# Kernel tuning notes

Measured on AMD Instinct MI355X. Metric: run time of the kernel, lower is better.

Reference implementation:

```python
import jax, jax.numpy as jnp
import numpy as np

N, E, G = 20480, 163840, 512          # nodes, edges, graphs
D, H, R, L = 128, 4, 8, 4             # embed dim, heads, relations, layers
HK = H * D                            # heads * out_channels (RGATConv internal width)
BOARD_WIDTH = 7
NEG_SLOPE = 0.2                       # RGATConv leaky_relu slope


def setup_inputs() -> dict:
    key = jax.random.key(0)
    ks = jax.random.split(key, 12)
    s_in = 1.0 / np.sqrt(D)
    s_att = 1.0 / np.sqrt(HK)
    return {
        "x_nodes": jax.random.randint(ks[0], (N,), 0, 3),
        "edge_index": jax.random.randint(ks[1], (2, E), 0, N),
        "edge_type": jax.random.randint(ks[2], (E,), 0, R),
        "batch": jnp.arange(N) // (N // G),  # G graphs of N//G nodes each
        "emb": jax.random.normal(ks[3], (3, D), jnp.float32),
        "W": jax.random.normal(ks[4], (L, R, D, HK), jnp.float32) * s_in,
        "Q": jax.random.normal(ks[5], (L, HK, H), jnp.float32) * s_att,
        "K": jax.random.normal(ks[6], (L, HK, H), jnp.float32) * s_att,
        "B": jnp.zeros((L, D), jnp.float32),
        "fc1_w": jax.random.normal(ks[7], (D, 64), jnp.float32) * s_in,
        "fc1_b": jnp.zeros((64,), jnp.float32),
        "pol_w": jax.random.normal(ks[8], (64, BOARD_WIDTH), jnp.float32) * 0.125,
        "pol_b": jnp.zeros((BOARD_WIDTH,), jnp.float32),
        "val_w": jax.random.normal(ks[9], (64, 1), jnp.float32) * 0.125,
        "val_b": jnp.zeros((1,), jnp.float32),
    }


def _rgat_layer(x, W, Q, Km, b, src, dst, etype):
    # RGATConv, additive-self-attention, across-relation softmax, concat=False.
    x_all = jnp.einsum('nd,rdk->nrk', x, W)          # [N,R,HK] per-relation transform
    q_all = jnp.einsum('nrk,kh->nrh', x_all, Q)      # [N,R,H]
    k_all = jnp.einsum('nrk,kh->nrh', x_all, Km)     # [N,R,H]
    alpha = jax.nn.leaky_relu(q_all[dst, etype] + k_all[src, etype], NEG_SLOPE)  # [E,H]
    # segment softmax over destination nodes (across all relations)
    amax = jax.lax.stop_gradient(jax.ops.segment_max(alpha, dst, num_segments=N))
    ex = jnp.exp(alpha - amax[dst])
    denom = jax.ops.segment_sum(ex, dst, num_segments=N)
    a = ex / (denom[dst] + 1e-16)                    # [E,H]
    msg = x_all[src, etype].reshape(E, H, D) * a[:, :, None]   # [E,H,D]
    agg = jax.ops.segment_sum(msg.reshape(E, HK), dst, num_segments=N)
    out = agg.reshape(N, H, D).mean(axis=1) + b      # head-mean (concat=False) + bias
    return jax.nn.relu(out)


def reference(x_nodes, edge_index, edge_type, batch, emb, W, Q, K, B,
              fc1_w, fc1_b, pol_w, pol_b, val_w, val_b):
    src, dst = edge_index[0], edge_index[1]
    x = emb[x_nodes]                                  # [N,D]
    for l in range(L):
        x = _rgat_layer(x, W[l], Q[l], K[l], B[l], src, dst, edge_type)
    cnt = jax.ops.segment_sum(jnp.ones((N,), x.dtype), batch, num_segments=G)
    pooled = jax.ops.segment_sum(x, batch, num_segments=G) / jnp.maximum(cnt, 1.0)[:, None]
    h = jax.nn.relu(pooled @ fc1_w + fc1_b)           # [G,64]
    policy = h @ pol_w + pol_b                        # [G,BOARD_WIDTH]
    value = jnp.tanh(h @ val_w + val_b)               # [G,1]
    return policy, value
```

## Files before the change

### kernel.cpp

```cpp
#include <hip/hip_runtime.h>
#include <cstdint>
#include <cstddef>

constexpr int N_  = 20480;
constexpr int E_  = 163840;
constexpr int G_  = 512;
constexpr int D_  = 128;
constexpr int H_  = 4;
constexpr int R_  = 8;
constexpr int L_  = 4;
constexpr int HK_ = 512;
constexpr int NPG_ = N_ / G_;

typedef short short8 __attribute__((ext_vector_type(8)));
typedef float f32x4 __attribute__((ext_vector_type(4)));
typedef unsigned short u16;
typedef unsigned int u32;

__device__ inline u16 bfr(float f) {
  u32 u = __builtin_bit_cast(u32, f);
  return (u16)((u + 0x7fffu + ((u >> 16) & 1u)) >> 16);
}
__device__ inline float bf2f(u32 lo16) { return __builtin_bit_cast(float, lo16 << 16); }
__device__ inline float lrelu(float v) { return v >= 0.f ? v : 0.2f * v; }

__global__ void k_zero_i(int* __restrict__ p, int n) {
  int i = blockIdx.x * blockDim.x + threadIdx.x;
  if (i < n) p[i] = 0;
}

__global__ void k_count_rel(const int* __restrict__ dst, const int* __restrict__ et,
                            int* __restrict__ counts) {
  int e = blockIdx.x * blockDim.x + threadIdx.x;
  if (e < E_) atomicAdd(&counts[et[e] * N_ + dst[e]], 1);
}
__global__ void k_count_dst(const int* __restrict__ dst, int* __restrict__ counts) {
  int e = blockIdx.x * blockDim.x + threadIdx.x;
  if (e < E_) atomicAdd(&counts[dst[e]], 1);
}
__global__ void k_bsum(const int* __restrict__ c, int* __restrict__ bsum) {
  int t = threadIdx.x;
  const int4 v = *(const int4*)&c[blockIdx.x * 1024 + t * 4];
  int s = v.x + v.y + v.z + v.w;
#pragma unroll
  for (int o = 32; o; o >>= 1) s += __shfl_down(s, o, 64);
  __shared__ int ws_[4];
  if ((t & 63) == 0) ws_[t >> 6] = s;
  __syncthreads();
  if (t == 0) bsum[blockIdx.x] = ws_[0] + ws_[1] + ws_[2] + ws_[3];
}
__global__ void k_bscan(int* __restrict__ bsum, int nb, int* __restrict__ tot_out) {
  __shared__ int sh[512];
  int t = threadIdx.x;
  if (t < nb) sh[t] = bsum[t];
  __syncthreads();
  if (t == 0) {
    int run = 0;
    for (int i = 0; i < nb; ++i) { int v = sh[i]; sh[i] = run; run += v; }
    tot_out[0] = run;
  }
  __syncthreads();
  if (t < nb) bsum[t] = sh[t];
}
__global__ void k_scan3(const int* __restrict__ c, const int* __restrict__ bsum,
                        int* __restrict__ indptr, int* __restrict__ cursor) {
  __shared__ int ts[256];
  int t = threadIdx.x;
  int base = blockIdx.x * 1024 + t * 4;
  const int4 v = *(const int4*)&c[base];
  int s0 = v.x, s01 = v.x + v.y, s012 = s01 + v.z, s = s012 + v.w;
  ts[t] = s;
  __syncthreads();
#pragma unroll
  for (int o = 1; o < 256; o <<= 1) {
    int add = (t >= o) ? ts[t - o] : 0;
    __syncthreads();
    ts[t] += add;
    __syncthreads();
  }
  int off = bsum[blockIdx.x] + (t ? ts[t - 1] : 0);
  int4 o4 = make_int4(off, off + s0, off + s01, off + s012);
  *(int4*)&indptr[base] = o4;
  *(int4*)&cursor[base] = o4;
}
__global__ void k_scatter_rel(const int* __restrict__ dst, const int* __restrict__ et,
                              const int* __restrict__ src, int* __restrict__ cursor,
                              int* __restrict__ esort, int* __restrict__ slotOf,
                              int* __restrict__ srcR) {
  int e = blockIdx.x * blockDim.x + threadIdx.x;
  if (e < E_) {
    int p = atomicAdd(&cursor[et[e] * N_ + dst[e]], 1);
    esort[p] = e;
    slotOf[e] = p;
    srcR[p] = src[e];
  }
}
__global__ void k_scatter_dst(const int* __restrict__ dst, int* __restrict__ cursor,
                              int* __restrict__ esort) {
  int e = blockIdx.x * blockDim.x + threadIdx.x;
  if (e < E_) {
    int p = atomicAdd(&cursor[dst[e]], 1);
    esort[p] = e;
  }
}
__global__ void k_padbase(const int* __restrict__ indptrR, int* __restrict__ padBase) {
  if (threadIdx.x == 0 && blockIdx.x == 0) {
    int cum = 0;
    for (int r = 0; r < R_; ++r) {
      padBase[r] = cum;
      int cnt = indptrR[(r + 1) * N_] - indptrR[r * N_];
      cum += (cnt + 63) & ~63;
    }
    padBase[R_] = cum;
  }
}

__global__ void k_embed(const int* __restrict__ xn, const float* __restrict__ emb,
                        float* __restrict__ x, u16* __restrict__ xb) {
  int i = blockIdx.x * blockDim.x + threadIdx.x;
  if (i < N_ * D_) {
    int n = i >> 7, d = i & 127;
    float v = emb[xn[n] * D_ + d];
    x[i] = v;
    xb[i] = bfr(v);
  }
}

__global__ __launch_bounds__(256) void k_wqk_all(const float* __restrict__ W,
                                                 const float* __restrict__ Q,
                                                 const float* __restrict__ Km,
                                                 float* __restrict__ WQK) {
  int gw = (blockIdx.x * 256 + threadIdx.x) >> 6;
  int lane = threadIdx.x & 63;
  int d = gw & 127, r = (gw >> 7) & 7, l = gw >> 10;
  const float* wrow = W + (((size_t)l * R_ + r) * D_ + d) * HK_;
  const float* Ql = Q + (size_t)l * HK_ * H_;
  const float* Kl = Km + (size_t)l * HK_ * H_;
  float acc[8] = {0.f, 0.f, 0.f, 0.f, 0.f, 0.f, 0.f, 0.f};
#pragma unroll
  for (int it = 0; it < 8; ++it) {
    int k = it * 64 + lane;
    float w = wrow[k];
    const float4 qv = *(const float4*)&Ql[k * 4];
    const float4 kv = *(const float4*)&Kl[k * 4];
    acc[0] += w * qv.x; acc[1] += w * qv.y; acc[2] += w * qv.z; acc[3] += w * qv.w;
    acc[4] += w * kv.x; acc[5] += w * kv.y; acc[6] += w * kv.z; acc[7] += w * kv.w;
  }
#pragma unroll
  for (int o = 32; o; o >>= 1)
#pragma unroll
    for (int j = 0; j < 8; ++j) acc[j] += __shfl_down(acc[j], o, 64);
  if (lane == 0) {
#pragma unroll
    for (int h = 0; h < 4; ++h) {
      WQK[((size_t)l * D_ + d) * 64 + r * 4 + h] = acc[h];
      WQK[((size_t)l * D_ + d) * 64 + 32 + r * 4 + h] = acc[4 + h];
    }
  }
}

__global__ __launch_bounds__(256) void k_qk(const float* __restrict__ x,
                                            const float* __restrict__ WQK,
                                            float* __restrict__ q,
                                            float* __restrict__ kk) {
  __shared__ float xs[32][129];
  __shared__ float wq[128][64];
  const int t = threadIdx.x;
  const int n0 = blockIdx.x * 32;
#pragma unroll
  for (int p = 0; p < 4; ++p) {
    int idx = t + p * 256;
    int row = idx >> 5, c4 = (idx & 31) * 4;
    const float4 v = *(const float4*)&x[(size_t)(n0 + row) * D_ + c4];
    xs[row][c4 + 0] = v.x; xs[row][c4 + 1] = v.y;
    xs[row][c4 + 2] = v.z; xs[row][c4 + 3] = v.w;
  }
#pragma unroll
  for (int p = 0; p < 8; ++p) {
    int idx = t + p * 256;
    int row = idx >> 4, c4 = (idx & 15) * 4;
    *(float4*)&wq[row][c4] = *(const float4*)&WQK[row * 64 + c4];
  }
  __syncthreads();
  const int node = t >> 3, cq = t & 7;
  float s[8];
#pragma unroll
  for (int j = 0; j < 8; ++j) s[j] = 0.f;
  for (int k = 0; k < 128; ++k) {
    float xv = xs[node][k];
#pragma unroll
    for (int j = 0; j < 8; ++j) s[j] = fmaf(xv, wq[k][cq * 8 + j], s[j]);
  }
#pragma unroll
  for (int j = 0; j < 8; ++j) {
    int c = cq * 8 + j;
    if (c < 32) q[(size_t)(n0 + node) * 32 + c] = s[j];
    else        kk[(size_t)(n0 + node) * 32 + (c - 32)] = s[j];
  }
}

__global__ __launch_bounds__(256) void k_attn(
    const int* __restrict__ ipN, const int* __restrict__ esD,
    const int* __restrict__ src, const int* __restrict__ et,
    const float* __restrict__ q, const float* __restrict__ kk,
    const int* __restrict__ slotOf, float* __restrict__ aw) {
  int n = blockIdx.x * 4 + (threadIdx.x >> 6);
  int lane = threadIdx.x & 63;
  int j0 = ipN[n], j1 = ipN[n + 1];
  int deg = j1 - j0;
  if (deg == 0) return;
  int h = lane & 3;
  int nch = (deg + 15) >> 4;
  float m = -3.4e38f;
  for (int c = 0; c < nch; ++c) {
    int ei = c * 16 + (lane >> 2);
    if (ei < deg) {
      int e = esD[j0 + ei];
      int r = et[e];
      float a = lrelu(q[(size_t)n * 32 + r * 4 + h] + kk[(size_t)src[e] * 32 + r * 4 + h]);
      m = fmaxf(m, a);
    }
  }
#pragma unroll
  for (int o = 4; o < 64; o <<= 1) m = fmaxf(m, __shfl_xor(m, o, 64));
  float s = 0.f;
  for (int c = 0; c < nch; ++c) {
    int ei = c * 16 + (lane >> 2);
    if (ei < deg) {
      int e = esD[j0 + ei];
      int r = et[e];
      float a = lrelu(q[(size_t)n * 32 + r * 4 + h] + kk[(size_t)src[e] * 32 + r * 4 + h]);
      float ex = expf(a - m);
      s += ex;
      aw[(size_t)slotOf[e] * 4 + h] = ex;
    }
  }
#pragma unroll
  for (int o = 4; o < 64; o <<= 1) s += __shfl_xor(s, o, 64);
  float inv = 0.25f / (s + 1e-16f);
  for (int c = 0; c < nch; ++c) {
    int ei = c * 16 + (lane >> 2);
    if (ei < deg) {
      int e = esD[j0 + ei];
      aw[(size_t)slotOf[e] * 4 + h] *= inv;
    }
  }
}

__global__ void k_cvt_w_all(const float* __restrict__ W, u16* __restrict__ wt) {
  __shared__ u16 tile[64][65];
  const int z = blockIdx.z, k0 = blockIdx.y * 64, c0 = blockIdx.x * 64;
  const int t = threadIdx.x;
  const int tk = t >> 4, tc4 = (t & 15) * 4;
  const float* Wz = W + (size_t)z * D_ * HK_;
  u16* wz = wt + (size_t)z * HK_ * D_;
#pragma unroll
  for (int p = 0; p < 4; ++p) {
    int krow = tk + p * 16;
    const float4 v = *(const float4*)&Wz[(size_t)(k0 + krow) * HK_ + c0 + tc4];
    tile[tc4 + 0][krow] = bfr(v.x);
    tile[tc4 + 1][krow] = bfr(v.y);
    tile[tc4 + 2][krow] = bfr(v.z);
    tile[tc4 + 3][krow] = bfr(v.w);
  }
  __syncthreads();
#pragma unroll
  for (int p = 0; p < 4; ++p) {
    int crow = tk + p * 16;
    uint2 o;
    o.x = (u32)tile[crow][tc4 + 0] | ((u32)tile[crow][tc4 + 1] << 16);
    o.y = (u32)tile[crow][tc4 + 2] | ((u32)tile[crow][tc4 + 3] << 16);
    *(uint2*)&wz[(size_t)(c0 + crow) * D_ + k0 + tc4] = o;
  }
}

__global__ __launch_bounds__(512, 2) void k_edge4(
    const u16* __restrict__ xb, const u16* __restrict__ wt,
    const int* __restrict__ indptrR, const int* __restrict__ padBase,
    const int* __restrict__ srcR, const float* __restrict__ aw,
    u16* __restrict__ m) {
  __shared__ u16 atile[64 * 128];
  __shared__ float awl[2][64][4];
  __shared__ int srcl[2][64];
  const int t = threadIdx.x;
  const int r = blockIdx.x >> 5;
  const int sub = blockIdx.x & 31;
  const int ip0 = indptrR[r * N_];
  const int cnt = indptrR[(r + 1) * N_] - ip0;
  const int nt = (cnt + 63) >> 6;
  const int pb = padBase[r];
  const u16* wrp = wt + (size_t)r * HK_ * D_;
  const int wid = t >> 6, lane = t & 63;
  const int l15 = lane & 15, l4 = lane >> 4;
  short8 breg[4][4];
#pragma unroll
  for (int ks = 0; ks < 4; ++ks)
#pragma unroll
    for (int h = 0; h < 4; ++h) {
      int c = (wid + 8 * h) * 16 + l15;
      breg[ks][h] = *(const short8*)(wrp + (size_t)c * 128 + ks * 32 + l4 * 8);
    }
  if (sub < nt && t < 64) {
    int lidx = sub * 64 + t;
    if (lidx < cnt) {
      srcl[0][t] = srcR[ip0 + lidx];
      *(float4*)awl[0][t] = *(const float4*)(aw + (size_t)(ip0 + lidx) * 4);
    } else {
      srcl[0][t] = 0;
      *(float4*)awl[0][t] = make_float4(0.f, 0.f, 0.f, 0.f);
    }
  }
  __syncthreads();
  uint4 pa[2];
  if (sub < nt) {
#pragma unroll
    for (int p = 0; p < 2; ++p) {
      int idx = t + p * 512;
      pa[p] = *(const uint4*)(xb + (size_t)srcl[0][idx >> 4] * 128 + (idx & 15) * 8);
    }
  }
  int cur = 0;
  for (int tile = sub; tile < nt; tile += 32) {
    const int nxt = cur ^ 1;
    const int ntile = tile + 32;
#pragma unroll
    for (int p = 0; p < 2; ++p) {
      int idx = t + p * 512;
      int row = idx >> 4, seg = idx & 15;
      *(uint4*)((char*)atile + row * 256 + ((seg * 16) ^ ((row & 7) << 4))) = pa[p];
    }
    if (ntile < nt && t < 64) {
      int lidx = ntile * 64 + t;
      if (lidx < cnt) {
        srcl[nxt][t] = srcR[ip0 + lidx];
        *(float4*)awl[nxt][t] = *(const float4*)(aw + (size_t)(ip0 + lidx) * 4);
      } else {
        srcl[nxt][t] = 0;
        *(float4*)awl[nxt][t] = make_float4(0.f, 0.f, 0.f, 0.f);
      }
    }
    __syncthreads();
    if (ntile < nt) {
#pragma unroll
      for (int p = 0; p < 2; ++p) {
        int idx = t + p * 512;
        pa[p] = *(const uint4*)(xb + (size_t)srcl[nxt][idx >> 4] * 128 + (idx & 15) * 8);
      }
    }
    f32x4 acc[4][4];
#pragma unroll
    for (int i = 0; i < 4; ++i)
#pragma unroll
      for (int h = 0; h < 4; ++h) acc[i][h] = (f32x4){0.f, 0.f, 0.f, 0.f};
#pragma unroll
    for (int ks = 0; ks < 4; ++ks) {
      short8 av[4];
#pragma unroll
      for (int i = 0; i < 4; ++i) {
        int row = i * 16 + l15;
        av[i] = *(const short8*)((char*)atile + row * 256 +
                  ((l4 * 16 + ks * 64) ^ ((row & 7) << 4)));
      }
#pragma unroll
      for (int i = 0; i < 4; ++i)
#pragma unroll
        for (int h = 0; h < 4; ++h)
          acc[i][h] = __builtin_amdgcn_mfma_f32_16x16x32_bf16(breg[ks][h], av[i],
                                                              acc[i][h], 0, 0, 0);
    }
#pragma unroll
    for (int i = 0; i < 4; ++i) {
      int row = i * 16 + l15;
      const float4 awf = *(const float4*)awl[cur][row];
      float v0 = awf.x * acc[i][0][0] + awf.y * acc[i][1][0] + awf.z * acc[i][2][0] + awf.w * acc[i][3][0];
      float v1 = awf.x * acc[i][0][1] + awf.y * acc[i][1][1] + awf.z * acc[i][2][1] + awf.w * acc[i][3][1];
      float v2 = awf.x * acc[i][0][2] + awf.y * acc[i][1][2] + awf.z * acc[i][2][2] + awf.w * acc[i][3][2];
      float v3 = awf.x * acc[i][0][3] + awf.y * acc[i][1][3] + awf.z * acc[i][2][3] + awf.w * acc[i][3][3];
      uint2 o;
      o.x = (u32)bfr(v0) | ((u32)bfr(v1) << 16);
      o.y = (u32)bfr(v2) | ((u32)bfr(v3) << 16);
      *(uint2*)(m + (size_t)(pb + tile * 64 + row) * 128 + wid * 16 + l4 * 4) = o;
    }
    __syncthreads();
    cur = nxt;
  }
}

__global__ __launch_bounds__(256) void k_agg2(
    const int* __restrict__ indptrR, const int* __restrict__ padBase,
    const u16* __restrict__ m, const float* __restrict__ Bl,
    float* __restrict__ xout, u16* __restrict__ xbout) {
  int n = blockIdx.x * 4 + (threadIdx.x >> 6);
  int lane = threadIdx.x & 63;
  float s0 = 0.f, s1 = 0.f;
#pragma unroll
  for (int r = 0; r < R_; ++r) {
    int ip0 = indptrR[r * N_];
    int j0 = indptrR[r * N_ + n], j1 = indptrR[r * N_ + n + 1];
    int base = padBase[r] + (j0 - ip0);
    for (int j = 0; j < j1 - j0; ++j) {
      u32 v = *((const u32*)(m + (size_t)(base + j) * 128) + lane);
      s0 += bf2f(v & 0xffffu);
      s1 += bf2f(v >> 16);
    }
  }
  float2 o;
  o.x = fmaxf(s0 + Bl[2 * lane], 0.f);
  o.y = fmaxf(s1 + Bl[2 * lane + 1], 0.f);
  *((float2*)(xout + (size_t)n * D_) + lane) = o;
  ((u32*)(xbout + (size_t)n * D_))[lane] = (u32)bfr(o.x) | ((u32)bfr(o.y) << 16);
}

__global__ void k_pool(const float* __restrict__ x, float* __restrict__ pooled) {
  int i = blockIdx.x * blockDim.x + threadIdx.x;
  if (i >= G_ * D_) return;
  int d = i & 127, g = i >> 7;
  float s = 0.f;
  for (int j = 0; j < NPG_; ++j) s += x[(size_t)(g * NPG_ + j) * D_ + d];
  pooled[i] = s * (1.0f / NPG_);
}

__global__ void k_head(const float* __restrict__ pooled, const float* __restrict__ fc1w,
                       const float* __restrict__ fc1b, const float* __restrict__ polw,
                       const float* __restrict__ polb, const float* __restrict__ valw,
                       const float* __restrict__ valb, float* __restrict__ out) {
  int g = blockIdx.x;
  int t = threadIdx.x;
  __shared__ float hb[64];
  const float* p = pooled + (size_t)g * D_;
  float s = fc1b[t];
  for (int d = 0; d < D_; ++d) s += p[d] * fc1w[d * 64 + t];
  hb[t] = fmaxf(s, 0.f);
  __syncthreads();
  if (t < 7) {
    float s2 = polb[t];
    for (int j = 0; j < 64; ++j) s2 += hb[j] * polw[j * 7 + t];
    out[g * 7 + t] = s2;
  } else if (t == 7) {
    float s2 = valb[0];
    for (int j = 0; j < 64; ++j) s2 += hb[j] * valw[j];
    out[G_ * 7 + g] = tanhf(s2);
  }
}

extern "C" void kernel_launch(void* const* d_in, const int* in_sizes, int n_in,
                              void* d_out, int out_size, void* d_ws, size_t ws_size,
                              hipStream_t stream) {
  (void)in_sizes; (void)n_in; (void)out_size;
  const int*   x_nodes = (const int*)d_in[0];
  const int*   eidx    = (const int*)d_in[1];
  const int*   etype   = (const int*)d_in[2];
  const float* emb     = (const float*)d_in[4];
  const float* W       = (const float*)d_in[5];
  const float* Q       = (const float*)d_in[6];
  const float* Km      = (const float*)d_in[7];
  const float* B       = (const float*)d_in[8];
  const float* fc1w    = (const float*)d_in[9];
  const float* fc1b    = (const float*)d_in[10];
  const float* polw    = (const float*)d_in[11];
  const float* polb    = (const float*)d_in[12];
  const float* valw    = (const float*)d_in[13];
  const float* valb    = (const float*)d_in[14];
  float* out = (float*)d_out;
  const int* srcA = eidx;
  const int* dstA = eidx + E_;

  char* p = (char*)d_ws;
  size_t used = 0;
  auto carve = [&](size_t bytes) {
    char* q = p;
    size_t adv = (bytes + 255) & ~(size_t)255;
    p += adv;
    used += adv;
    return q;
  };
  float* x_cur  = (float*)carve((size_t)N_ * D_ * 4);
  float* x_nxt  = (float*)carve((size_t)N_ * D_ * 4);
  u16*   xbf    = (u16*)carve((size_t)N_ * D_ * 2);
  u16*   mbuf   = (u16*)carve((size_t)(E_ + 512) * D_ * 2);
  float* qbuf   = (float*)carve((size_t)N_ * 32 * 4);
  float* kbuf   = (float*)carve((size_t)N_ * 32 * 4);
  float* awbuf  = (float*)carve((size_t)E_ * H_ * 4);
  float* WQKb   = (float*)carve((size_t)L_ * D_ * 64 * 4);
  u16*   Wtb    = (u16*)carve((size_t)L_ * R_ * HK_ * D_ * 2);
  float* pooled = (float*)carve((size_t)G_ * D_ * 4);
  int* countsR  = (int*)carve((size_t)R_ * N_ * 4);
  int* cursorR  = (int*)carve((size_t)R_ * N_ * 4);
  int* indptrR  = (int*)carve((size_t)(R_ * N_ + 1) * 4);
  int* esortR   = (int*)carve((size_t)E_ * 4);
  int* slotOf   = (int*)carve((size_t)E_ * 4);
  int* srcR     = (int*)carve((size_t)E_ * 4);
  int* countsN  = (int*)carve((size_t)N_ * 4);
  int* cursorN  = (int*)carve((size_t)N_ * 4);
  int* indptrN  = (int*)carve((size_t)(N_ + 1) * 4);
  int* esortD   = (int*)carve((size_t)E_ * 4);
  int* padBase  = (int*)carve((size_t)(R_ + 1) * 4);
  int* bsum     = (int*)carve((size_t)512 * 4);
  if (used > ws_size) return;

  constexpr int RN = R_ * N_;
  constexpr int NBR = RN / 1024;
  constexpr int NBN = N_ / 1024;

  k_zero_i<<<(RN + 255) / 256, 256, 0, stream>>>(countsR, RN);
  k_zero_i<<<(N_ + 255) / 256, 256, 0, stream>>>(countsN, N_);
  k_count_rel<<<E_ / 256, 256, 0, stream>>>(dstA, etype, countsR);
  k_count_dst<<<E_ / 256, 256, 0, stream>>>(dstA, countsN);
  k_bsum<<<NBR, 256, 0, stream>>>(countsR, bsum);
  k_bscan<<<1, 512, 0, stream>>>(bsum, NBR, indptrR + RN);
  k_scan3<<<NBR, 256, 0, stream>>>(countsR, bsum, indptrR, cursorR);
  k_scatter_rel<<<E_ / 256, 256, 0, stream>>>(dstA, etype, srcA, cursorR, esortR,
                                              slotOf, srcR);
  k_bsum<<<NBN, 256, 0, stream>>>(countsN, bsum);
  k_bscan<<<1, 512, 0, stream>>>(bsum, NBN, indptrN + N_);
  k_scan3<<<NBN, 256, 0, stream>>>(countsN, bsum, indptrN, cursorN);
  k_scatter_dst<<<E_ / 256, 256, 0, stream>>>(dstA, cursorN, esortD);
  k_padbase<<<1, 64, 0, stream>>>(indptrR, padBase);
  k_embed<<<(N_ * D_) / 256, 256, 0, stream>>>(x_nodes, emb, x_cur, xbf);
  k_wqk_all<<<(L_ * R_ * D_ * 64) / 256, 256, 0, stream>>>(W, Q, Km, WQKb);
  k_cvt_w_all<<<dim3(HK_ / 64, D_ / 64, L_ * R_), 256, 0, stream>>>(W, Wtb);

  for (int l = 0; l < L_; ++l) {
    const float* Bl = B + (size_t)l * D_;
    k_qk<<<N_ / 32, 256, 0, stream>>>(x_cur, WQKb + (size_t)l * D_ * 64, qbuf, kbuf);
    k_attn<<<N_ / 4, 256, 0, stream>>>(indptrN, esortD, srcA, etype, qbuf, kbuf,
                                       slotOf, awbuf);
    k_edge4<<<R_ * 32, 512, 0, stream>>>(xbf, Wtb + (size_t)l * R_ * HK_ * D_,
                                         indptrR, padBase, srcR, awbuf, mbuf);
    k_agg2<<<N_ / 4, 256, 0, stream>>>(indptrR, padBase, mbuf, Bl, x_nxt, xbf);
    float* tmp = x_cur; x_cur = x_nxt; x_nxt = tmp;
  }

  k_pool<<<(G_ * D_) / 256, 256, 0, stream>>>(x_cur, pooled);
  k_head<<<G_, 64, 0, stream>>>(pooled, fc1w, fc1b, polw, polb, valw, valb, out);
}
```

Measured before the change: 528.8 us.

## Launch one block per 64-edge tile instead of persistent per-relation blocks

Replaces the persistent edge kernel, which used 32 blocks per relation looping over tiles with software-prefetched gathers, with a flat grid where each block handles exactly one padded 64-edge tile and finds its relation by scanning padBase. This is meant to raise parallelism from 256 blocks to about 2568 and to balance work across CUs. In exchange, every block reloads its relation's full weight slice into registers and there is no longer any overlap between the gather and the MFMA work within a block.

```diff
diff --git a/kernel.cpp b/kernel.cpp
--- a/kernel.cpp
+++ b/kernel.cpp
@@ -274,21 +274,22 @@
   }
 }
 
-__global__ __launch_bounds__(512, 2) void k_edge4(
+__global__ __launch_bounds__(512) void k_edge5(
     const u16* __restrict__ xb, const u16* __restrict__ wt,
     const int* __restrict__ indptrR, const int* __restrict__ padBase,
     const int* __restrict__ srcR, const float* __restrict__ aw,
     u16* __restrict__ m) {
   __shared__ u16 atile[64 * 128];
-  __shared__ float awl[2][64][4];
-  __shared__ int srcl[2][64];
+  __shared__ float awl[64][4];
+  __shared__ int srcl[64];
   const int t = threadIdx.x;
-  const int r = blockIdx.x >> 5;
-  const int sub = blockIdx.x & 31;
+  const int b64 = blockIdx.x * 64;
+  if (b64 >= padBase[R_]) return;
+  int r = 0;
+  while (b64 >= padBase[r + 1]) ++r;
   const int ip0 = indptrR[r * N_];
   const int cnt = indptrR[(r + 1) * N_] - ip0;
-  const int nt = (cnt + 63) >> 6;
-  const int pb = padBase[r];
+  const int local0 = b64 - padBase[r];
   const u16* wrp = wt + (size_t)r * HK_ * D_;
   const int wid = t >> 6, lane = t & 63;
   const int l15 = lane & 15, l4 = lane >> 4;
@@ -300,89 +301,58 @@
       int c = (wid + 8 * h) * 16 + l15;
       breg[ks][h] = *(const short8*)(wrp + (size_t)c * 128 + ks * 32 + l4 * 8);
     }
-  if (sub < nt && t < 64) {
-    int lidx = sub * 64 + t;
+  if (t < 64) {
+    int lidx = local0 + t;
     if (lidx < cnt) {
-      srcl[0][t] = srcR[ip0 + lidx];
-      *(float4*)awl[0][t] = *(const float4*)(aw + (size_t)(ip0 + lidx) * 4);
+      srcl[t] = srcR[ip0 + lidx];
+      *(float4*)awl[t] = *(const float4*)(aw + (size_t)(ip0 + lidx) * 4);
     } else {
-      srcl[0][t] = 0;
-      *(float4*)awl[0][t] = make_float4(0.f, 0.f, 0.f, 0.f);
-    }
-  }
-  __syncthreads();
-  uint4 pa[2];
-  if (sub < nt) {
-#pragma unroll
-    for (int p = 0; p < 2; ++p) {
-      int idx = t + p * 512;
-      pa[p] = *(const uint4*)(xb + (size_t)srcl[0][idx >> 4] * 128 + (idx & 15) * 8);
-    }
-  }
-  int cur = 0;
-  for (int tile = sub; tile < nt; tile += 32) {
-    const int nxt = cur ^ 1;
-    const int ntile = tile + 32;
-#pragma unroll
-    for (int p = 0; p < 2; ++p) {
-      int idx = t + p * 512;
-      int row = idx >> 4, seg = idx & 15;
-      *(uint4*)((char*)atile + row * 256 + ((seg * 16) ^ ((row & 7) << 4))) = pa[p];
-    }
-    if (ntile < nt && t < 64) {
-      int lidx = ntile * 64 + t;
-      if (lidx < cnt) {
-        srcl[nxt][t] = srcR[ip0 + lidx];
-        *(float4*)awl[nxt][t] = *(const float4*)(aw + (size_t)(ip0 + lidx) * 4);
-      } else {
-        srcl[nxt][t] = 0;
-        *(float4*)awl[nxt][t] = make_float4(0.f, 0.f, 0.f, 0.f);
-      }
-    }
-    __syncthreads();
-    if (ntile < nt) {
-#pragma unroll
-      for (int p = 0; p < 2; ++p) {
-        int idx = t + p * 512;
-        pa[p] = *(const uint4*)(xb + (size_t)srcl[nxt][idx >> 4] * 128 + (idx & 15) * 8);
-      }
-    }
-    f32x4 acc[4][4];
-#pragma unroll
-    for (int i = 0; i < 4; ++i)
-#pragma unroll
-      for (int h = 0; h < 4; ++h) acc[i][h] = (f32x4){0.f, 0.f, 0.f, 0.f};
-#pragma unroll
-    for (int ks = 0; ks < 4; ++ks) {
-      short8 av[4];
-#pragma unroll
-      for (int i = 0; i < 4; ++i) {
-        int row = i * 16 + l15;
-        av[i] = *(const short8*)((char*)atile + row * 256 +
-                  ((l4 * 16 + ks * 64) ^ ((row & 7) << 4)));
-      }
-#pragma unroll
-      for (int i = 0; i < 4; ++i)
-#pragma unroll
-        for (int h = 0; h < 4; ++h)
-          acc[i][h] = __builtin_amdgcn_mfma_f32_16x16x32_bf16(breg[ks][h], av[i],
-                                                              acc[i][h], 0, 0, 0);
-    }
+      srcl[t] = 0;
+      *(float4*)awl[t] = make_float4(0.f, 0.f, 0.f, 0.f);
+    }
+  }
+  __syncthreads();
+#pragma unroll
+  for (int p = 0; p < 2; ++p) {
+    int idx = t + p * 512;
+    int row = idx >> 4, seg = idx & 15;
+    uint4 v = *(const uint4*)(xb + (size_t)srcl[row] * 128 + seg * 8);
+    *(uint4*)((char*)atile + row * 256 + ((seg * 16) ^ ((row & 7) << 4))) = v;
+  }
+  __syncthreads();
+  f32x4 acc[4][4];
+#pragma unroll
+  for (int i = 0; i < 4; ++i)
+#pragma unroll
+    for (int h = 0; h < 4; ++h) acc[i][h] = (f32x4){0.f, 0.f, 0.f, 0.f};
+#pragma unroll
+  for (int ks = 0; ks < 4; ++ks) {
+    short8 av[4];
 #pragma unroll
     for (int i = 0; i < 4; ++i) {
       int row = i * 16 + l15;
-      const float4 awf = *(const float4*)awl[cur][row];
-      float v0 = awf.x * acc[i][0][0] + awf.y * acc[i][1][0] + awf.z * acc[i][2][0] + awf.w * acc[i][3][0];
-      float v1 = awf.x * acc[i][0][1] + awf.y * acc[i][1][1] + awf.z * acc[i][2][1] + awf.w * acc[i][3][1];
-      float v2 = awf.x * acc[i][0][2] + awf.y * acc[i][1][2] + awf.z * acc[i][2][2] + awf.w * acc[i][3][2];
-      float v3 = awf.x * acc[i][0][3] + awf.y * acc[i][1][3] + awf.z * acc[i][2][3] + awf.w * acc[i][3][3];
-      uint2 o;
-      o.x = (u32)bfr(v0) | ((u32)bfr(v1) << 16);
-      o.y = (u32)bfr(v2) | ((u32)bfr(v3) << 16);
-      *(uint2*)(m + (size_t)(pb + tile * 64 + row) * 128 + wid * 16 + l4 * 4) = o;
-    }
-    __syncthreads();
-    cur = nxt;
+      av[i] = *(const short8*)((char*)atile + row * 256 +
+                ((l4 * 16 + ks * 64) ^ ((row & 7) << 4)));
+    }
+#pragma unroll
+    for (int i = 0; i < 4; ++i)
+#pragma unroll
+      for (int h = 0; h < 4; ++h)
+        acc[i][h] = __builtin_amdgcn_mfma_f32_16x16x32_bf16(breg[ks][h], av[i],
+                                                            acc[i][h], 0, 0, 0);
+  }
+#pragma unroll
+  for (int i = 0; i < 4; ++i) {
+    int row = i * 16 + l15;
+    const float4 awf = *(const float4*)awl[row];
+    float v0 = awf.x * acc[i][0][0] + awf.y * acc[i][1][0] + awf.z * acc[i][2][0] + awf.w * acc[i][3][0];
+    float v1 = awf.x * acc[i][0][1] + awf.y * acc[i][1][1] + awf.z * acc[i][2][1] + awf.w * acc[i][3][1];
+    float v2 = awf.x * acc[i][0][2] + awf.y * acc[i][1][2] + awf.z * acc[i][2][2] + awf.w * acc[i][3][2];
+    float v3 = awf.x * acc[i][0][3] + awf.y * acc[i][1][3] + awf.z * acc[i][2][3] + awf.w * acc[i][3][3];
+    uint2 o;
+    o.x = (u32)bfr(v0) | ((u32)bfr(v1) << 16);
+    o.y = (u32)bfr(v2) | ((u32)bfr(v3) << 16);
+    *(uint2*)(m + (size_t)(b64 + row) * 128 + wid * 16 + l4 * 4) = o;
   }
 }
 
@@ -501,6 +471,7 @@
   constexpr int RN = R_ * N_;
   constexpr int NBR = RN / 1024;
   constexpr int NBN = N_ / 1024;
+  constexpr int EDGE_BLOCKS = E_ / 64 + R_;
 
   k_zero_i<<<(RN + 255) / 256, 256, 0, stream>>>(countsR, RN);
   k_zero_i<<<(N_ + 255) / 256, 256, 0, stream>>>(countsN, N_);
@@ -525,8 +496,8 @@
     k_qk<<<N_ / 32, 256, 0, stream>>>(x_cur, WQKb + (size_t)l * D_ * 64, qbuf, kbuf);
     k_attn<<<N_ / 4, 256, 0, stream>>>(indptrN, esortD, srcA, etype, qbuf, kbuf,
                                        slotOf, awbuf);
-    k_edge4<<<R_ * 32, 512, 0, stream>>>(xbf, Wtb + (size_t)l * R_ * HK_ * D_,
-                                         indptrR, padBase, srcR, awbuf, mbuf);
+    k_edge5<<<EDGE_BLOCKS, 512, 0, stream>>>(xbf, Wtb + (size_t)l * R_ * HK_ * D_,
+                                             indptrR, padBase, srcR, awbuf, mbuf);
     k_agg2<<<N_ / 4, 256, 0, stream>>>(indptrR, padBase, mbuf, Bl, x_nxt, xbf);
     float* tmp = x_cur; x_cur = x_nxt; x_nxt = tmp;
   }
```

New measurement: 544.1 us. 2.9% more time.
